# Kernel optimization log

Measured on AMD Instinct MI355X. Metric: run time of the kernel, lower is better.

## Reference

```python
import jax, jax.numpy as jnp
import numpy as np

POOL = 7        # output pooled size
SAMP = 2 * POOL # crop_and_resize sampling resolution (14)


def _bilinear_crop(feat, ys, xs):
    """feat [H,W,C]; ys,xs [N,S] sample coords in feature-map pixels -> [N,S,S,C]."""
    H, W, _ = feat.shape
    ys = jnp.clip(ys, 0.0, H - 1.0)
    xs = jnp.clip(xs, 0.0, W - 1.0)
    y0f = jnp.floor(ys); x0f = jnp.floor(xs)
    y0 = y0f.astype(jnp.int32); x0 = x0f.astype(jnp.int32)
    y1 = jnp.clip(y0 + 1, 0, H - 1); x1 = jnp.clip(x0 + 1, 0, W - 1)
    wy = (ys - y0f)[:, :, None, None]   # [N,S,1,1]
    wx = (xs - x0f)[:, None, :, None]   # [N,1,S,1]
    g = lambda yi, xi: feat[yi[:, :, None], xi[:, None, :]]  # [N,S,S,C]
    out = g(y0, x0) * (1 - wy) * (1 - wx)
    out = out + g(y0, x1) * (1 - wy) * wx
    out = out + g(y1, x0) * wy * (1 - wx)
    out = out + g(y1, x1) * wy * wx
    return out


def setup_inputs() -> dict:
    key = jax.random.key(0)
    k1, k2, k3, k4, k5 = jax.random.split(key, 5)
    Hf, Wf, C = 37, 50, 512
    N = 1000
    H_img, W_img = 600.0, 800.0
    inputs = jax.random.normal(k1, (1, Hf, Wf, C), dtype=jnp.float32)
    # random valid boxes (x1,y1,x2,y2) in image coords
    cx = jax.random.uniform(k2, (N,)) * W_img
    cy = jax.random.uniform(k3, (N,)) * H_img
    bw = jax.random.uniform(k4, (N,)) * 300.0 + 16.0
    bh = jax.random.uniform(k5, (N,)) * 300.0 + 16.0
    x1 = jnp.clip(cx - bw / 2, 0.0, W_img - 1.0)
    y1 = jnp.clip(cy - bh / 2, 0.0, H_img - 1.0)
    x2 = jnp.clip(cx + bw / 2, 0.0, W_img - 1.0)
    y2 = jnp.clip(cy + bh / 2, 0.0, H_img - 1.0)
    rois = jnp.stack([x1, y1, x2, y2], axis=1).astype(jnp.float32)
    im_size = jnp.array([600, 800], dtype=jnp.int32)  # (h, w)
    return {"inputs": inputs, "rois": rois, "im_size": im_size}


def reference(inputs, rois, im_size):
    feat = inputs[0]                       # [Hf, Wf, C]
    Hf, Wf, C = feat.shape
    h = im_size[0].astype(jnp.float32)
    w = im_size[1].astype(jnp.float32)
    # normalize boxes to [0,1] (y1, x1, y2, x2), as in roi_pool_tf
    ny1 = rois[:, 1] / h; nx1 = rois[:, 0] / w
    ny2 = rois[:, 3] / h; nx2 = rois[:, 2] / w
    # crop_and_resize sample grid (TF convention: endpoints at box corners)
    t = jnp.linspace(0.0, 1.0, SAMP, dtype=jnp.float32)          # [S]
    ys = (ny1[:, None] + (ny2 - ny1)[:, None] * t[None, :]) * (Hf - 1)  # [N,S]
    xs = (nx1[:, None] + (nx2 - nx1)[:, None] * t[None, :]) * (Wf - 1)  # [N,S]
    crops = _bilinear_crop(feat, ys, xs)   # [N,14,14,C]
    N = crops.shape[0]
    pooled = crops.reshape(N, POOL, 2, POOL, 2, C).max(axis=(2, 4))  # [N,7,7,C]
    return pooled
```

## Files before the change

### kernel.cpp

```cpp
#include <hip/hip_runtime.h>
#include <math.h>

#define HF 37
#define WF 50
#define CC 512
#define POOLD 7
#define SAMPD 14

typedef float nfloat4 __attribute__((ext_vector_type(4)));

__device__ __forceinline__ float4 lerp4(float4 a, float4 b, float t) {
    float4 r;
    r.x = a.x + t * (b.x - a.x);
    r.y = a.y + t * (b.y - a.y);
    r.z = a.z + t * (b.z - a.z);
    r.w = a.w + t * (b.w - a.w);
    return r;
}

__device__ __forceinline__ float4 max4(float4 a, float4 b) {
    float4 r;
    r.x = fmaxf(a.x, b.x);
    r.y = fmaxf(a.y, b.y);
    r.z = fmaxf(a.z, b.z);
    r.w = fmaxf(a.w, b.w);
    return r;
}

__device__ __forceinline__ void store_nt4(float* p, float4 v) {
    nfloat4 nv;
    nv.x = v.x; nv.y = v.y; nv.z = v.z; nv.w = v.w;
    __builtin_nontemporal_store(nv, (nfloat4*)p);
}

struct Raw { float4 a, b, c, d; };

template <int RC>
__device__ __forceinline__ Raw loadraw(const float* __restrict__ pbase, int col,
                                       int ro0, int ro1, int ro2, int ro3) {
    const float* p = pbase + (size_t)col * CC;
    Raw r;
    r.a = *(const float4*)(p + ro0);
    r.b = *(const float4*)(p + ro1);
    if (RC == 1) { r.c = *(const float4*)(p + ro3); }
    if (RC == 2) { r.c = *(const float4*)(p + ro2); r.d = *(const float4*)(p + ro3); }
    return r;
}

template <int RC>
__device__ __forceinline__ void vlerp(const Raw& r, float wya, float wyb,
                                      float4& va, float4& vb) {
    if (RC == 0)      { va = lerp4(r.a, r.b, wya); vb = lerp4(r.a, r.b, wyb); }
    else if (RC == 1) { va = lerp4(r.a, r.b, wya); vb = lerp4(r.b, r.c, wyb); }
    else              { va = lerp4(r.a, r.b, wya); vb = lerp4(r.c, r.d, wyb); }
}

template <int RC>
__device__ __forceinline__ void run_row(const float* __restrict__ pbase,
                                        float* __restrict__ obase,
                                        float nx1, float dx,
                                        int ro0, int ro1, int ro2, int ro3,
                                        float wya, float wyb)
{
    const float inv    = 1.0f / (float)(SAMPD - 1);
    const float wscale = (float)(WF - 1);
    constexpr int D     = (RC == 0) ? 3 : ((RC == 1) ? 2 : 1);
    constexpr int SLOTS = D + 1;

    Raw   ls[SLOTS], rs[SLOTS];
    float ws[SLOTS];

    float4 m0 = make_float4(-INFINITY, -INFINITY, -INFINITY, -INFINITY);

    #pragma unroll
    for (int i = 0; i < SAMPD + D; ++i) {
        if (i < SAMPD) {
            float tx  = (float)i * inv;
            float xs  = fmaf(dx, tx, nx1) * wscale;
            xs        = fminf(fmaxf(xs, 0.0f), wscale);
            float x0f = floorf(xs);
            int c0 = __builtin_amdgcn_readfirstlane((int)x0f);
            int c1 = min(c0 + 1, WF - 1);
            ws[i % SLOTS] = xs - x0f;
            ls[i % SLOTS] = loadraw<RC>(pbase, c0, ro0, ro1, ro2, ro3);
            rs[i % SLOTS] = loadraw<RC>(pbase, c1, ro0, ro1, ro2, ro3);
        }
        if (i >= D) {
            int k = i - D;
            int s = k % SLOTS;
            float4 va0, vb0, va1, vb1;
            vlerp<RC>(ls[s], wya, wyb, va0, vb0);
            vlerp<RC>(rs[s], wya, wyb, va1, vb1);
            float w  = ws[s];
            float4 sa = lerp4(va0, va1, w);
            float4 sb = lerp4(vb0, vb1, w);
            m0 = max4(m0, max4(sa, sb));
            if (k & 1) {
                store_nt4(obase + (size_t)(k >> 1) * CC, m0);
                m0 = make_float4(-INFINITY, -INFINITY, -INFINITY, -INFINITY);
            }
        }
    }
}

__global__ __launch_bounds__(128, 4) void roipool_kernel(
    const float* __restrict__ feat,
    const float* __restrict__ rois,
    const int*   __restrict__ im_size,
    float*       __restrict__ out,
    int N)
{
    int bid = blockIdx.x;
    int n   = bid / POOLD;
    int py  = bid - n * POOLD;
    if (n >= N) return;

    float h = (float)im_size[0];
    float w = (float)im_size[1];
    float4 box = *(const float4*)(rois + 4 * n);
    float ny1 = box.y / h, nx1 = box.x / w;
    float ny2 = box.w / h, nx2 = box.z / w;
    float dx = nx2 - nx1;

    const float inv = 1.0f / (float)(SAMPD - 1);

    float tya = (float)(2 * py) * inv;
    float tyb = (float)(2 * py + 1) * inv;
    float ysa = (ny1 + (ny2 - ny1) * tya) * (float)(HF - 1);
    float ysb = (ny1 + (ny2 - ny1) * tyb) * (float)(HF - 1);
    ysa = fminf(fmaxf(ysa, 0.0f), (float)(HF - 1));
    ysb = fminf(fmaxf(ysb, 0.0f), (float)(HF - 1));
    float y0fa = floorf(ysa);
    float y0fb = floorf(ysb);
    float wya = ysa - y0fa;
    float wyb = ysb - y0fb;
    int iya = __builtin_amdgcn_readfirstlane((int)y0fa);
    int iyb = __builtin_amdgcn_readfirstlane((int)y0fb);
    int iya1 = min(iya + 1, HF - 1);
    int iyb1 = min(iyb + 1, HF - 1);
    int ro0 = iya  * (WF * CC);
    int ro1 = iya1 * (WF * CC);
    int ro2 = iyb  * (WF * CC);
    int ro3 = iyb1 * (WF * CC);

    const float* pbase = feat + (size_t)threadIdx.x * 4;
    float* obase = out + ((size_t)(n * POOLD + py) * POOLD) * CC + (size_t)threadIdx.x * 4;

    if (ro2 == ro0) {
        run_row<0>(pbase, obase, nx1, dx, ro0, ro1, ro2, ro3, wya, wyb);
    } else if (ro2 == ro1) {
        run_row<1>(pbase, obase, nx1, dx, ro0, ro1, ro2, ro3, wya, wyb);
    } else {
        run_row<2>(pbase, obase, nx1, dx, ro0, ro1, ro2, ro3, wya, wyb);
    }
}

extern "C" void kernel_launch(void* const* d_in, const int* in_sizes, int n_in,
                              void* d_out, int out_size, void* d_ws, size_t ws_size,
                              hipStream_t stream) {
    const float* feat    = (const float*)d_in[0];
    const float* rois    = (const float*)d_in[1];
    const int*   im_size = (const int*)d_in[2];
    float* out = (float*)d_out;

    int N = in_sizes[1] / 4;
    int nblocks = N * POOLD;
    roipool_kernel<<<nblocks, 128, 0, stream>>>(feat, rois, im_size, out, N);
}
```

Before: 136.5 us.

## Restructure ROI pooling to sweep feature columns with separable vertical interpolation reuse

Each block now handles a whole ROI for one half of the channels, instead of one pooled row for all channels. For each feature column in the ROI's span it interpolates all 14 vertical sample rows once, then reuses the previous and current column results for every horizontal sample that falls between them. This is meant to cut redundant feature loads and repeated vertical lerps across pooled rows. In exchange there are fewer blocks (2N instead of 7N), narrower float2 accesses, more registers per thread, and a data-dependent sequential loop over columns that may lower memory-level parallelism.

```diff
diff --git a/kernel.cpp b/kernel.cpp
--- a/kernel.cpp
+++ b/kernel.cpp
@@ -7,151 +7,129 @@
 #define POOLD 7
 #define SAMPD 14
 
-typedef float nfloat4 __attribute__((ext_vector_type(4)));
+typedef float nfloat2 __attribute__((ext_vector_type(2)));
 
-__device__ __forceinline__ float4 lerp4(float4 a, float4 b, float t) {
-    float4 r;
-    r.x = a.x + t * (b.x - a.x);
-    r.y = a.y + t * (b.y - a.y);
-    r.z = a.z + t * (b.z - a.z);
-    r.w = a.w + t * (b.w - a.w);
-    return r;
+__device__ __forceinline__ float2 lerp2(float2 a, float2 b, float t) {
+    float2 r; r.x = a.x + t * (b.x - a.x); r.y = a.y + t * (b.y - a.y); return r;
+}
+__device__ __forceinline__ float2 max2(float2 a, float2 b) {
+    float2 r; r.x = fmaxf(a.x, b.x); r.y = fmaxf(a.y, b.y); return r;
+}
+__device__ __forceinline__ void store_nt2(float* p, float2 v) {
+    nfloat2 nv; nv.x = v.x; nv.y = v.y;
+    __builtin_nontemporal_store(nv, (nfloat2*)p);
 }
 
-__device__ __forceinline__ float4 max4(float4 a, float4 b) {
-    float4 r;
-    r.x = fmaxf(a.x, b.x);
-    r.y = fmaxf(a.y, b.y);
-    r.z = fmaxf(a.z, b.z);
-    r.w = fmaxf(a.w, b.w);
-    return r;
-}
-
-__device__ __forceinline__ void store_nt4(float* p, float4 v) {
-    nfloat4 nv;
-    nv.x = v.x; nv.y = v.y; nv.z = v.z; nv.w = v.w;
-    __builtin_nontemporal_store(nv, (nfloat4*)p);
-}
-
-struct Raw { float4 a, b, c, d; };
-
-template <int RC>
-__device__ __forceinline__ Raw loadraw(const float* __restrict__ pbase, int col,
-                                       int ro0, int ro1, int ro2, int ro3) {
-    const float* p = pbase + (size_t)col * CC;
-    Raw r;
-    r.a = *(const float4*)(p + ro0);
-    r.b = *(const float4*)(p + ro1);
-    if (RC == 1) { r.c = *(const float4*)(p + ro3); }
-    if (RC == 2) { r.c = *(const float4*)(p + ro2); r.d = *(const float4*)(p + ro3); }
-    return r;
-}
-
-template <int RC>
-__device__ __forceinline__ void vlerp(const Raw& r, float wya, float wyb,
-                                      float4& va, float4& vb) {
-    if (RC == 0)      { va = lerp4(r.a, r.b, wya); vb = lerp4(r.a, r.b, wyb); }
-    else if (RC == 1) { va = lerp4(r.a, r.b, wya); vb = lerp4(r.b, r.c, wyb); }
-    else              { va = lerp4(r.a, r.b, wya); vb = lerp4(r.c, r.d, wyb); }
-}
-
-template <int RC>
-__device__ __forceinline__ void run_row(const float* __restrict__ pbase,
-                                        float* __restrict__ obase,
-                                        float nx1, float dx,
-                                        int ro0, int ro1, int ro2, int ro3,
-                                        float wya, float wyb)
-{
-    const float inv    = 1.0f / (float)(SAMPD - 1);
-    const float wscale = (float)(WF - 1);
-    constexpr int D     = (RC == 0) ? 3 : ((RC == 1) ? 2 : 1);
-    constexpr int SLOTS = D + 1;
-
-    Raw   ls[SLOTS], rs[SLOTS];
-    float ws[SLOTS];
-
-    float4 m0 = make_float4(-INFINITY, -INFINITY, -INFINITY, -INFINITY);
-
-    #pragma unroll
-    for (int i = 0; i < SAMPD + D; ++i) {
-        if (i < SAMPD) {
-            float tx  = (float)i * inv;
-            float xs  = fmaf(dx, tx, nx1) * wscale;
-            xs        = fminf(fmaxf(xs, 0.0f), wscale);
-            float x0f = floorf(xs);
-            int c0 = __builtin_amdgcn_readfirstlane((int)x0f);
-            int c1 = min(c0 + 1, WF - 1);
-            ws[i % SLOTS] = xs - x0f;
-            ls[i % SLOTS] = loadraw<RC>(pbase, c0, ro0, ro1, ro2, ro3);
-            rs[i % SLOTS] = loadraw<RC>(pbase, c1, ro0, ro1, ro2, ro3);
-        }
-        if (i >= D) {
-            int k = i - D;
-            int s = k % SLOTS;
-            float4 va0, vb0, va1, vb1;
-            vlerp<RC>(ls[s], wya, wyb, va0, vb0);
-            vlerp<RC>(rs[s], wya, wyb, va1, vb1);
-            float w  = ws[s];
-            float4 sa = lerp4(va0, va1, w);
-            float4 sb = lerp4(vb0, vb1, w);
-            m0 = max4(m0, max4(sa, sb));
-            if (k & 1) {
-                store_nt4(obase + (size_t)(k >> 1) * CC, m0);
-                m0 = make_float4(-INFINITY, -INFINITY, -INFINITY, -INFINITY);
-            }
-        }
-    }
-}
-
-__global__ __launch_bounds__(128, 4) void roipool_kernel(
+__global__ __launch_bounds__(128, 3) void roipool_kernel(
     const float* __restrict__ feat,
     const float* __restrict__ rois,
     const int*   __restrict__ im_size,
     float*       __restrict__ out,
     int N)
 {
-    int bid = blockIdx.x;
-    int n   = bid / POOLD;
-    int py  = bid - n * POOLD;
+    int bid   = blockIdx.x;
+    int n     = bid >> 1;
+    int chalf = bid & 1;
     if (n >= N) return;
+
+    const int choff = chalf * (CC / 2) + (int)threadIdx.x * 2;
 
     float h = (float)im_size[0];
     float w = (float)im_size[1];
     float4 box = *(const float4*)(rois + 4 * n);
     float ny1 = box.y / h, nx1 = box.x / w;
     float ny2 = box.w / h, nx2 = box.z / w;
-    float dx = nx2 - nx1;
-
+    float dy = ny2 - ny1, dx = nx2 - nx1;
     const float inv = 1.0f / (float)(SAMPD - 1);
 
-    float tya = (float)(2 * py) * inv;
-    float tyb = (float)(2 * py + 1) * inv;
-    float ysa = (ny1 + (ny2 - ny1) * tya) * (float)(HF - 1);
-    float ysb = (ny1 + (ny2 - ny1) * tyb) * (float)(HF - 1);
-    ysa = fminf(fmaxf(ysa, 0.0f), (float)(HF - 1));
-    ysb = fminf(fmaxf(ysb, 0.0f), (float)(HF - 1));
-    float y0fa = floorf(ysa);
-    float y0fb = floorf(ysb);
-    float wya = ysa - y0fa;
-    float wyb = ysb - y0fb;
-    int iya = __builtin_amdgcn_readfirstlane((int)y0fa);
-    int iyb = __builtin_amdgcn_readfirstlane((int)y0fb);
-    int iya1 = min(iya + 1, HF - 1);
-    int iyb1 = min(iyb + 1, HF - 1);
-    int ro0 = iya  * (WF * CC);
-    int ro1 = iya1 * (WF * CC);
-    int ro2 = iyb  * (WF * CC);
-    int ro3 = iyb1 * (WF * CC);
+    int   y1s[SAMPD];
+    float wye[SAMPD];
+    int rmin = 0, rmax = 0;
+    #pragma unroll
+    for (int i = 0; i < SAMPD; ++i) {
+        float t   = (float)i * inv;
+        float ys  = fmaf(dy, t, ny1) * (float)(HF - 1);
+        ys        = fminf(fmaxf(ys, 0.0f), (float)(HF - 1));
+        float y0f = floorf(ys);
+        int   y0  = __builtin_amdgcn_readfirstlane((int)y0f);
+        int   y1  = min(y0 + 1, HF - 1);
+        wye[i] = (y1 == y0) ? 1.0f : (ys - y0f);
+        y1s[i] = y1;
+        if (i == 0)         rmin = y0;
+        if (i == SAMPD - 1) rmax = y1;
+    }
 
-    const float* pbase = feat + (size_t)threadIdx.x * 4;
-    float* obase = out + ((size_t)(n * POOLD + py) * POOLD) * CC + (size_t)threadIdx.x * 4;
+    auto sampx = [&](int j, int& pc, float& wxe) {
+        float tx  = (float)j * inv;
+        float xs  = fmaf(dx, tx, nx1) * (float)(WF - 1);
+        xs        = fminf(fmaxf(xs, 0.0f), (float)(WF - 1));
+        float x0f = floorf(xs);
+        int   ci  = __builtin_amdgcn_readfirstlane((int)x0f);
+        float wx  = xs - x0f;
+        if (ci >= WF - 1) { pc = WF - 1; wxe = 1.0f; }
+        else              { pc = ci + 1; wxe = wx; }
+    };
+    int pc0, pcl; float wdum;
+    sampx(0, pc0, wdum);
+    sampx(SAMPD - 1, pcl, wdum);
+    int cfirst = pc0 - 1;
+    int clast  = pcl;
 
-    if (ro2 == ro0) {
-        run_row<0>(pbase, obase, nx1, dx, ro0, ro1, ro2, ro3, wya, wyb);
-    } else if (ro2 == ro1) {
-        run_row<1>(pbase, obase, nx1, dx, ro0, ro1, ro2, ro3, wya, wyb);
-    } else {
-        run_row<2>(pbase, obase, nx1, dx, ro0, ro1, ro2, ro3, wya, wyb);
+    float2 Hp[SAMPD], Hc[SAMPD];
+    float2 m[POOLD];
+    #pragma unroll
+    for (int p = 0; p < POOLD; ++p) m[p] = make_float2(-INFINITY, -INFINITY);
+
+    const float* fbase = feat + choff;
+    float*       obase = out + (size_t)n * (POOLD * POOLD) * CC + choff;
+
+    int j = 0;
+    for (int c = cfirst; ; ++c) {
+        {
+            const float* colp = fbase + (size_t)c * CC;
+            int rcur = rmin;
+            float2 prv, cur, nxt;
+            cur = *(const float2*)(colp + (size_t)rmin * (WF * CC));
+            nxt = (rmin + 1 <= rmax)
+                      ? *(const float2*)(colp + (size_t)(rmin + 1) * (WF * CC))
+                      : cur;
+            prv = cur;
+            #pragma unroll
+            for (int i = 0; i < SAMPD; ++i) {
+                while (rcur < y1s[i]) {
+                    prv = cur; cur = nxt; ++rcur;
+                    if (rcur + 1 <= rmax)
+                        nxt = *(const float2*)(colp + (size_t)(rcur + 1) * (WF * CC));
+                }
+                Hc[i] = lerp2(prv, cur, wye[i]);
+            }
+        }
+        if (c > cfirst) {
+            for (;;) {
+                if (j >= SAMPD) break;
+                int pc; float wxe;
+                sampx(j, pc, wxe);
+                if (pc > c) break;
+                #pragma unroll
+                for (int p = 0; p < POOLD; ++p) {
+                    float2 v = max2(lerp2(Hp[2 * p],     Hc[2 * p],     wxe),
+                                    lerp2(Hp[2 * p + 1], Hc[2 * p + 1], wxe));
+                    m[p] = max2(m[p], v);
+                }
+                if (j & 1) {
+                    int px = j >> 1;
+                    #pragma unroll
+                    for (int p = 0; p < POOLD; ++p) {
+                        store_nt2(obase + (size_t)(p * POOLD + px) * CC, m[p]);
+                        m[p] = make_float2(-INFINITY, -INFINITY);
+                    }
+                }
+                ++j;
+            }
+        }
+        if (c == clast) break;
+        #pragma unroll
+        for (int i = 0; i < SAMPD; ++i) Hp[i] = Hc[i];
     }
 }
 
@@ -164,6 +142,6 @@
     float* out = (float*)d_out;
 
     int N = in_sizes[1] / 4;
-    int nblocks = N * POOLD;
+    int nblocks = 2 * N;
     roipool_kernel<<<nblocks, 128, 0, stream>>>(feat, rois, im_size, out, N);
 }
```

Result: slower. 167.8 us (+23.0%).
